# Optimization experiments

Measured on AMD Instinct MI355X. Metric: run time of the kernel, lower is better.

## Reference

```python
import jax, jax.numpy as jnp
import numpy as np

B, L, E, H, D = 4, 8192, 1024, 64, 2  # batch, seq, embed, heads, head_dim(=expand_ratio)
F_DIM = H * D  # forget_dim = 128
LOWER_BOUND = 0.0


def setup_inputs() -> dict:
    key = jax.random.key(0)
    k0, k1, k2, k3, k4 = jax.random.split(key, 5)
    s = E ** -0.5
    x = jax.random.normal(k0, (B, L, E), jnp.float32)
    Wq = jax.random.normal(k1, (E, F_DIM), jnp.float32) * s
    Wf = jax.random.normal(k2, (E, F_DIM), jnp.float32) * s
    Wi = jax.random.normal(k3, (E, F_DIM), jnp.float32) * s
    Wo = jax.random.normal(k4, (F_DIM, E), jnp.float32) * (F_DIM ** -0.5)
    return {"x": x, "Wq": Wq, "Wf": Wf, "Wi": Wi, "Wo": Wo}


def _split_heads(t):
    # b l (h d) -> b h l d
    return t.reshape(B, L, H, D).transpose(0, 2, 1, 3)


def _fused_recurrent_gla(q, k, v, g):
    # q,k,v,g: [b,h,l,d]; state S: [b,h,dk,dv]
    scale = D ** -0.5
    qs = jnp.moveaxis(q * scale, 2, 0)  # [l,b,h,d]
    ks = jnp.moveaxis(k, 2, 0)
    vs = jnp.moveaxis(v, 2, 0)
    gs = jnp.moveaxis(g, 2, 0)

    def step(S, inp):
        qt, kt, vt, gt = inp  # each [b,h,d]
        S = jnp.exp(gt)[..., None] * S + kt[..., None] * vt[..., None, :]
        o = jnp.einsum('bhk,bhkv->bhv', qt, S)
        return S, o

    S0 = jnp.zeros((B, H, D, D), q.dtype)
    _, o = jax.lax.scan(step, S0, (qs, ks, vs, gs))  # o: [l,b,h,d]
    return jnp.moveaxis(o, 0, 2)  # [b,h,l,d]


def reference(x, Wq, Wf, Wi, Wo):
    q = jax.nn.gelu(x @ Wq, approximate=False)  # torch nn.GELU default is exact erf
    f = x @ Wf
    g = LOWER_BOUND + (1.0 - LOWER_BOUND) * jax.nn.sigmoid(f)
    i = x @ Wi
    k = 1.0 - g
    g = jnp.log(g + 1e-6)
    q, k, v, g = map(_split_heads, (q, k, i, g))
    o = _fused_recurrent_gla(q, k, v, g)  # [b,h,l,d]
    o = o.transpose(0, 2, 1, 3).reshape(B, L, F_DIM)  # b h l d -> b l (h d)
    return jnp.tanh(o) @ Wo
```

## Files before the change

kernel.cpp:

```cpp
#include <hip/hip_runtime.h>
#include <hip/hip_bf16.h>


typedef __bf16 bf16x8 __attribute__((ext_vector_type(8)));
typedef float f32x4 __attribute__((ext_vector_type(4)));

__device__ __forceinline__ void async16(const void* g, void* l) {
  __builtin_amdgcn_global_load_lds(
      (const __attribute__((address_space(1))) unsigned int*)g,
      (__attribute__((address_space(3))) unsigned int*)l, 16, 0, 0);
}

__device__ __forceinline__ unsigned short f2bf(float f) {
  __hip_bfloat16 h = __float2bfloat16(f);
  return *reinterpret_cast<unsigned short*>(&h);
}
__device__ __forceinline__ float bf2f(unsigned short u) {
  union { unsigned int i; float f; } x; x.i = ((unsigned int)u) << 16; return x.f;
}

__global__ __launch_bounds__(256) void prep_w(
    const float* __restrict__ Wq, const float* __restrict__ Wf,
    const float* __restrict__ Wi, const float* __restrict__ Wo,
    unsigned short* __restrict__ WT, unsigned short* __restrict__ WoT) {
  int idx = blockIdx.x * 256 + threadIdx.x;
  if (idx < 393216) {
    int which = idx >> 17;
    int r = idx & 131071;
    int k = r >> 7, n = r & 127;
    const float* W = (which == 0) ? Wq : ((which == 1) ? Wf : Wi);
    WT[which * 131072 + n * 1024 + k] = f2bf(W[r]);
  } else {
    int r = idx - 393216;
    int k = r >> 10, n = r & 1023;
    WoT[n * 128 + k] = f2bf(Wo[r]);
  }
}

__global__ __launch_bounds__(256) void gemm1_kernel(
    const float* __restrict__ X, const unsigned short* __restrict__ WTall,
    unsigned short* __restrict__ qb, unsigned short* __restrict__ kb,
    unsigned short* __restrict__ vb, float* __restrict__ af) {
  __shared__ __align__(128) char smem[32768];
  const int t = threadIdx.x;
  const int lane = t & 63, w = t >> 6;
  const int quad = lane >> 4, c15 = lane & 15;
  const int wm = w >> 1, wn = w & 1;
  const int sel = blockIdx.x;
  const int row0 = blockIdx.y * 128;
  const unsigned short* Wt = WTall + (size_t)sel * 131072;

  const int lrow = t >> 3;
  const int ch = (t & 7) ^ (lrow & 7);
  const int ar = t >> 4;
  const int ac = (t & 15) >> 1;
  const int ah = t & 1;
  const int ak = (t & 15) * 4;

  f32x4 acc[4][4];
#pragma unroll
  for (int i = 0; i < 4; i++)
#pragma unroll
    for (int j = 0; j < 4; j++) acc[i][j] = (f32x4){0.f, 0.f, 0.f, 0.f};

  for (int kt = 0; kt < 16; ++kt) {
    float4 av[8];
#pragma unroll
    for (int i = 0; i < 8; ++i)
      av[i] = *(const float4*)(X + (size_t)(row0 + i * 16 + ar) * 1024 + kt * 64 + ak);
    __syncthreads();
#pragma unroll
    for (int c = 0; c < 4; ++c)
      async16(Wt + (size_t)(c * 32 + lrow) * 1024 + kt * 64 + ch * 8,
              smem + 16384 + c * 4096 + w * 1024);
#pragma unroll
    for (int i = 0; i < 8; ++i) {
      const int r = i * 16 + ar;
      short4 s4;
      s4.x = (short)f2bf(av[i].x); s4.y = (short)f2bf(av[i].y);
      s4.z = (short)f2bf(av[i].z); s4.w = (short)f2bf(av[i].w);
      *(short4*)(smem + r * 128 + ((ac ^ (r & 7)) << 4) + ah * 8) = s4;
    }
    __syncthreads();
#pragma unroll
    for (int ks = 0; ks < 2; ++ks) {
      bf16x8 afr[4], bfr[4];
      const int ck = ks * 4 + quad;
#pragma unroll
      for (int mi = 0; mi < 4; ++mi) {
        const int m = wm * 64 + mi * 16 + c15;
        afr[mi] = *(const bf16x8*)(smem + m * 128 + ((ck ^ (m & 7)) << 4));
      }
#pragma unroll
      for (int ni = 0; ni < 4; ++ni) {
        const int n = wn * 64 + ni * 16 + c15;
        bfr[ni] = *(const bf16x8*)(smem + 16384 + n * 128 + ((ck ^ (n & 7)) << 4));
      }
#pragma unroll
      for (int mi = 0; mi < 4; ++mi)
#pragma unroll
        for (int ni = 0; ni < 4; ++ni)
          acc[mi][ni] = __builtin_amdgcn_mfma_f32_16x16x32_bf16(afr[mi], bfr[ni], acc[mi][ni], 0, 0, 0);
    }
  }
#pragma unroll
  for (int mi = 0; mi < 4; ++mi) {
#pragma unroll
    for (int ni = 0; ni < 4; ++ni) {
#pragma unroll
      for (int r2 = 0; r2 < 4; ++r2) {
        float val = acc[mi][ni][r2];
        const int m = wm * 64 + mi * 16 + quad * 4 + r2;
        const int n = wn * 64 + ni * 16 + c15;
        const int grow = row0 + m;
        const int bb = grow >> 13, l = grow & 8191;
        const int h = n >> 1, d = n & 1;
        const size_t idx = (size_t)(bb * 64 + h) * 16384 + l * 2 + d;
        if (sel == 0) {
          qb[idx] = f2bf(0.5f * val * (1.f + erff(val * 0.70710678118654752f)));
        } else if (sel == 1) {
          float s  = 1.f / (1.f + expf(-val));
          float ks = 1.f / (1.f + expf(val));
          kb[idx] = f2bf(ks);
          af[idx] = s + 1e-6f;
        } else {
          vb[idx] = f2bf(val);
        }
      }
    }
  }
}

struct C6 { float A0, A1, B00, B01, B10, B11; };
__device__ __forceinline__ C6 comb(const C6& p, const C6& c) {
  C6 r;
  r.A0 = p.A0 * c.A0; r.A1 = p.A1 * c.A1;
  r.B00 = c.A0 * p.B00 + c.B00; r.B01 = c.A0 * p.B01 + c.B01;
  r.B10 = c.A1 * p.B10 + c.B10; r.B11 = c.A1 * p.B11 + c.B11;
  return r;
}
__device__ __forceinline__ C6 shflup(const C6& c, unsigned d) {
  C6 r;
  r.A0 = __shfl_up(c.A0, d); r.A1 = __shfl_up(c.A1, d);
  r.B00 = __shfl_up(c.B00, d); r.B01 = __shfl_up(c.B01, d);
  r.B10 = __shfl_up(c.B10, d); r.B11 = __shfl_up(c.B11, d);
  return r;
}
__device__ __forceinline__ void ld8bf(const unsigned short* p, float* dst) {
  union { int4 v; unsigned short u[8]; } x;
  x.v = *(const int4*)p;
#pragma unroll
  for (int j = 0; j < 8; ++j) dst[j] = bf2f(x.u[j]);
}

__global__ __launch_bounds__(256) void scan_kernel(
    const unsigned short* __restrict__ qb, const unsigned short* __restrict__ kb,
    const unsigned short* __restrict__ vb, const float* __restrict__ af,
    unsigned short* __restrict__ ob) {
  const int t = threadIdx.x, lane = t & 63, w = t >> 6;
  __shared__ C6 cw[2][4];
  const size_t base = (size_t)blockIdx.x * 16384;
  float P00 = 0.f, P01 = 0.f, P10 = 0.f, P11 = 0.f;

  for (int i = 0; i < 4; ++i) {
    const int e0 = i * 4096 + t * 16;
    float q[16], k[16], v[16], a[16];
    ld8bf(qb + base + e0, q); ld8bf(qb + base + e0 + 8, q + 8);
    ld8bf(kb + base + e0, k); ld8bf(kb + base + e0 + 8, k + 8);
    ld8bf(vb + base + e0, v); ld8bf(vb + base + e0 + 8, v + 8);
#pragma unroll
    for (int j = 0; j < 4; j++) ((float4*)a)[j] = ((const float4*)(af + base + e0))[j];

    C6 c = {1.f, 1.f, 0.f, 0.f, 0.f, 0.f};
#pragma unroll
    for (int j = 0; j < 8; j++) {
      float a0 = a[2 * j], a1 = a[2 * j + 1], k0 = k[2 * j], k1 = k[2 * j + 1];
      float v0 = v[2 * j], v1 = v[2 * j + 1];
      c.A0 *= a0; c.A1 *= a1;
      c.B00 = a0 * c.B00 + k0 * v0; c.B01 = a0 * c.B01 + k0 * v1;
      c.B10 = a1 * c.B10 + k1 * v0; c.B11 = a1 * c.B11 + k1 * v1;
    }
    C6 inc = c;
#pragma unroll
    for (int d = 1; d < 64; d <<= 1) {
      C6 u = shflup(inc, d);
      if (lane >= d) inc = comb(u, inc);
    }
    if (lane == 63) cw[i & 1][w] = inc;
    __syncthreads();
    C6 wp = {1.f, 1.f, 0.f, 0.f, 0.f, 0.f};
    for (int ww = 0; ww < w; ++ww) wp = comb(wp, cw[i & 1][ww]);
    C6 tot = cw[i & 1][0];
    for (int ww = 1; ww < 4; ++ww) tot = comb(tot, cw[i & 1][ww]);
    C6 ex = shflup(inc, 1);
    if (lane == 0) ex = (C6){1.f, 1.f, 0.f, 0.f, 0.f, 0.f};
    C6 te = comb(wp, ex);
    float S00 = te.A0 * P00 + te.B00, S01 = te.A0 * P01 + te.B01;
    float S10 = te.A1 * P10 + te.B10, S11 = te.A1 * P11 + te.B11;
    union { int4 v[2]; unsigned short u[16]; } ou;
#pragma unroll
    for (int j = 0; j < 8; j++) {
      float a0 = a[2 * j], a1 = a[2 * j + 1], k0 = k[2 * j], k1 = k[2 * j + 1];
      float v0 = v[2 * j], v1 = v[2 * j + 1];
      S00 = a0 * S00 + k0 * v0; S01 = a0 * S01 + k0 * v1;
      S10 = a1 * S10 + k1 * v0; S11 = a1 * S11 + k1 * v1;
      float o0 = 0.70710678118654752f * (q[2 * j] * S00 + q[2 * j + 1] * S10);
      float o1 = 0.70710678118654752f * (q[2 * j] * S01 + q[2 * j + 1] * S11);
      ou.u[2 * j] = f2bf(tanhf(o0));
      ou.u[2 * j + 1] = f2bf(tanhf(o1));
    }
    *(int4*)(ob + base + e0) = ou.v[0];
    *(int4*)(ob + base + e0 + 8) = ou.v[1];
    float nP00 = tot.A0 * P00 + tot.B00, nP01 = tot.A0 * P01 + tot.B01;
    float nP10 = tot.A1 * P10 + tot.B10, nP11 = tot.A1 * P11 + tot.B11;
    P00 = nP00; P01 = nP01; P10 = nP10; P11 = nP11;
  }
}

__global__ __launch_bounds__(256) void gemm2_kernel(
    const unsigned short* __restrict__ ob, const unsigned short* __restrict__ WoT,
    float* __restrict__ out) {
  __shared__ __align__(128) char smem[49152];
  const int t = threadIdx.x, lane = t & 63, w = t >> 6;
  const int quad = lane >> 4, c15 = lane & 15;
  const int n0 = blockIdx.x * 128;
  const int row0 = blockIdx.y * 64;
  const int bb = row0 >> 13;
  const int l0 = row0 & 8191;
  {
    const int h = t & 63, q2 = t >> 6;
    const unsigned short* g = ob + (size_t)(bb * 64 + h) * 16384 + (size_t)(l0 + q2 * 16) * 2;
    const int cbase = h >> 2;
    const int ioff = (h & 3) * 4;
#pragma unroll
    for (int i = 0; i < 4; i++) {
      union { int4 v; unsigned int u[4]; } d4;
      d4.v = *(const int4*)(g + i * 8);
#pragma unroll
      for (int jj = 0; jj < 4; jj++) {
        const int lrr = q2 * 16 + i * 4 + jj;
        *(unsigned int*)(smem + lrr * 256 + ((cbase ^ (lrr & 15)) << 4) + ioff) = d4.u[jj];
      }
    }
  }
  {
    const int rr = t >> 4;
    const int ch = (t & 15) ^ rr;
#pragma unroll
    for (int c = 0; c < 8; c++) {
      async16(WoT + (size_t)(n0 + c * 16 + rr) * 128 + ch * 8,
              smem + 16384 + c * 4096 + w * 1024);
    }
  }
  __syncthreads();
  f32x4 acc[4][2];
#pragma unroll
  for (int i = 0; i < 4; i++) { acc[i][0] = (f32x4){0.f,0.f,0.f,0.f}; acc[i][1] = (f32x4){0.f,0.f,0.f,0.f}; }
#pragma unroll
  for (int ks = 0; ks < 4; ++ks) {
    bf16x8 afr[4], bfr[2];
    const int ck = ks * 4 + quad;
#pragma unroll
    for (int mi = 0; mi < 4; ++mi) {
      const int m = mi * 16 + c15;
      afr[mi] = *(const bf16x8*)(smem + m * 256 + ((ck ^ (m & 15)) << 4));
    }
#pragma unroll
    for (int ni = 0; ni < 2; ++ni) {
      const int n = w * 32 + ni * 16 + c15;
      bfr[ni] = *(const bf16x8*)(smem + 16384 + n * 256 + ((ck ^ (n & 15)) << 4));
    }
#pragma unroll
    for (int mi = 0; mi < 4; ++mi)
#pragma unroll
      for (int ni = 0; ni < 2; ++ni)
        acc[mi][ni] = __builtin_amdgcn_mfma_f32_16x16x32_bf16(afr[mi], bfr[ni], acc[mi][ni], 0, 0, 0);
  }
#pragma unroll
  for (int mi = 0; mi < 4; ++mi)
#pragma unroll
    for (int ni = 0; ni < 2; ++ni)
#pragma unroll
      for (int r2 = 0; r2 < 4; ++r2) {
        const int m = mi * 16 + quad * 4 + r2;
        const int n = n0 + w * 32 + ni * 16 + c15;
        out[(size_t)(row0 + m) * 1024 + n] = acc[mi][ni][r2];
      }
}

extern "C" void kernel_launch(void* const* d_in, const int* in_sizes, int n_in,
                              void* d_out, int out_size, void* d_ws, size_t ws_size,
                              hipStream_t stream) {
  const float* x  = (const float*)d_in[0];
  const float* Wq = (const float*)d_in[1];
  const float* Wf = (const float*)d_in[2];
  const float* Wi = (const float*)d_in[3];
  const float* Wo = (const float*)d_in[4];
  float* out = (float*)d_out;
  char* ws = (char*)d_ws;

  unsigned short* WT  = (unsigned short*)(ws);
  unsigned short* WoT = (unsigned short*)(ws + 786432);
  unsigned short* qb  = (unsigned short*)(ws + 1048576);
  unsigned short* kb  = (unsigned short*)(ws + 1048576 + 8388608);
  unsigned short* vb  = (unsigned short*)(ws + 1048576 + 16777216);
  float*          af  = (float*)(ws + 1048576 + 25165824);
  unsigned short* ob  = (unsigned short*)(ws + 1048576 + 41943040);

  prep_w<<<2048, 256, 0, stream>>>(Wq, Wf, Wi, Wo, WT, WoT);
  gemm1_kernel<<<dim3(3, 256), 256, 0, stream>>>(x, WT, qb, kb, vb, af);
  scan_kernel<<<256, 256, 0, stream>>>(qb, kb, vb, af, ob);
  gemm2_kernel<<<dim3(8, 512), 256, 0, stream>>>(ob, WoT, out);
}
```

Baseline: 346.2 us.

## Fuse three projection GEMMs per block so X tile is loaded once

```diff
diff --git a/kernel.cpp b/kernel.cpp
--- a/kernel.cpp
+++ b/kernel.cpp
@@ -37,94 +37,104 @@
   }
 }
 
-__global__ __launch_bounds__(256) void gemm1_kernel(
+__global__ __launch_bounds__(256, 2) void gemm1_kernel(
     const float* __restrict__ X, const unsigned short* __restrict__ WTall,
     unsigned short* __restrict__ qb, unsigned short* __restrict__ kb,
     unsigned short* __restrict__ vb, float* __restrict__ af) {
-  __shared__ __align__(128) char smem[32768];
+  __shared__ __align__(128) char smem[57344];
   const int t = threadIdx.x;
   const int lane = t & 63, w = t >> 6;
   const int quad = lane >> 4, c15 = lane & 15;
   const int wm = w >> 1, wn = w & 1;
-  const int sel = blockIdx.x;
-  const int row0 = blockIdx.y * 128;
-  const unsigned short* Wt = WTall + (size_t)sel * 131072;
-
-  const int lrow = t >> 3;
-  const int ch = (t & 7) ^ (lrow & 7);
-  const int ar = t >> 4;
-  const int ac = (t & 15) >> 1;
-  const int ah = t & 1;
-  const int ak = (t & 15) * 4;
-
-  f32x4 acc[4][4];
-#pragma unroll
-  for (int i = 0; i < 4; i++)
-#pragma unroll
-    for (int j = 0; j < 4; j++) acc[i][j] = (f32x4){0.f, 0.f, 0.f, 0.f};
+  const int row0 = blockIdx.x * 64;
+
+  const int br = t >> 3;
+  const int bch = (t & 7) ^ (br & 7);
+  const int ar = t >> 2;
+  const int akf = (t & 3) * 16;
+  const int ac0 = (t & 3) * 2;
+
+  f32x4 acc[3][2][4];
+#pragma unroll
+  for (int s = 0; s < 3; ++s)
+#pragma unroll
+    for (int i = 0; i < 2; ++i)
+#pragma unroll
+      for (int j = 0; j < 4; ++j) acc[s][i][j] = (f32x4){0.f, 0.f, 0.f, 0.f};
 
   for (int kt = 0; kt < 16; ++kt) {
-    float4 av[8];
-#pragma unroll
-    for (int i = 0; i < 8; ++i)
-      av[i] = *(const float4*)(X + (size_t)(row0 + i * 16 + ar) * 1024 + kt * 64 + ak);
+    float4 av[4];
+    const float* xp = X + (size_t)(row0 + ar) * 1024 + kt * 64 + akf;
+#pragma unroll
+    for (int i = 0; i < 4; ++i) av[i] = *(const float4*)(xp + i * 4);
     __syncthreads();
 #pragma unroll
-    for (int c = 0; c < 4; ++c)
-      async16(Wt + (size_t)(c * 32 + lrow) * 1024 + kt * 64 + ch * 8,
-              smem + 16384 + c * 4096 + w * 1024);
-#pragma unroll
-    for (int i = 0; i < 8; ++i) {
-      const int r = i * 16 + ar;
-      short4 s4;
-      s4.x = (short)f2bf(av[i].x); s4.y = (short)f2bf(av[i].y);
-      s4.z = (short)f2bf(av[i].z); s4.w = (short)f2bf(av[i].w);
-      *(short4*)(smem + r * 128 + ((ac ^ (r & 7)) << 4) + ah * 8) = s4;
+    for (int s = 0; s < 3; ++s)
+#pragma unroll
+      for (int c = 0; c < 4; ++c)
+        async16(WTall + (size_t)s * 131072 + (size_t)(c * 32 + br) * 1024 + kt * 64 + bch * 8,
+                smem + 8192 + s * 16384 + c * 4096 + w * 1024);
+    {
+      union { unsigned short u[16]; int4 v[2]; } p;
+#pragma unroll
+      for (int i = 0; i < 4; ++i) {
+        p.u[4 * i + 0] = f2bf(av[i].x); p.u[4 * i + 1] = f2bf(av[i].y);
+        p.u[4 * i + 2] = f2bf(av[i].z); p.u[4 * i + 3] = f2bf(av[i].w);
+      }
+      *(int4*)(smem + ar * 128 + (((ac0 + 0) ^ (ar & 7)) << 4)) = p.v[0];
+      *(int4*)(smem + ar * 128 + (((ac0 + 1) ^ (ar & 7)) << 4)) = p.v[1];
     }
     __syncthreads();
 #pragma unroll
     for (int ks = 0; ks < 2; ++ks) {
-      bf16x8 afr[4], bfr[4];
       const int ck = ks * 4 + quad;
-#pragma unroll
-      for (int mi = 0; mi < 4; ++mi) {
-        const int m = wm * 64 + mi * 16 + c15;
+      bf16x8 afr[2], bfr[3][4];
+#pragma unroll
+      for (int mi = 0; mi < 2; ++mi) {
+        const int m = wm * 32 + mi * 16 + c15;
         afr[mi] = *(const bf16x8*)(smem + m * 128 + ((ck ^ (m & 7)) << 4));
       }
 #pragma unroll
+      for (int s = 0; s < 3; ++s)
+#pragma unroll
+        for (int ni = 0; ni < 4; ++ni) {
+          const int n = wn * 64 + ni * 16 + c15;
+          bfr[s][ni] = *(const bf16x8*)(smem + 8192 + s * 16384 + n * 128 + ((ck ^ (n & 7)) << 4));
+        }
+#pragma unroll
+      for (int s = 0; s < 3; ++s)
+#pragma unroll
+        for (int mi = 0; mi < 2; ++mi)
+#pragma unroll
+          for (int ni = 0; ni < 4; ++ni)
+            acc[s][mi][ni] = __builtin_amdgcn_mfma_f32_16x16x32_bf16(afr[mi], bfr[s][ni], acc[s][mi][ni], 0, 0, 0);
+    }
+  }
+#pragma unroll
+  for (int s = 0; s < 3; ++s) {
+#pragma unroll
+    for (int mi = 0; mi < 2; ++mi) {
+#pragma unroll
       for (int ni = 0; ni < 4; ++ni) {
-        const int n = wn * 64 + ni * 16 + c15;
-        bfr[ni] = *(const bf16x8*)(smem + 16384 + n * 128 + ((ck ^ (n & 7)) << 4));
-      }
-#pragma unroll
-      for (int mi = 0; mi < 4; ++mi)
-#pragma unroll
-        for (int ni = 0; ni < 4; ++ni)
-          acc[mi][ni] = __builtin_amdgcn_mfma_f32_16x16x32_bf16(afr[mi], bfr[ni], acc[mi][ni], 0, 0, 0);
-    }
-  }
-#pragma unroll
-  for (int mi = 0; mi < 4; ++mi) {
-#pragma unroll
-    for (int ni = 0; ni < 4; ++ni) {
-#pragma unroll
-      for (int r2 = 0; r2 < 4; ++r2) {
-        float val = acc[mi][ni][r2];
-        const int m = wm * 64 + mi * 16 + quad * 4 + r2;
-        const int n = wn * 64 + ni * 16 + c15;
-        const int grow = row0 + m;
-        const int bb = grow >> 13, l = grow & 8191;
-        const int h = n >> 1, d = n & 1;
-        const size_t idx = (size_t)(bb * 64 + h) * 16384 + l * 2 + d;
-        if (sel == 0) {
-          qb[idx] = f2bf(0.5f * val * (1.f + erff(val * 0.70710678118654752f)));
-        } else if (sel == 1) {
-          float s  = 1.f / (1.f + expf(-val));
-          float ks = 1.f / (1.f + expf(val));
-          kb[idx] = f2bf(ks);
-          af[idx] = s + 1e-6f;
-        } else {
-          vb[idx] = f2bf(val);
+#pragma unroll
+        for (int r2 = 0; r2 < 4; ++r2) {
+          float val = acc[s][mi][ni][r2];
+          const int m = wm * 32 + mi * 16 + quad * 4 + r2;
+          const int n = wn * 64 + ni * 16 + c15;
+          const int grow = row0 + m;
+          const int bb = grow >> 13, l = grow & 8191;
+          const int h = n >> 1, d = n & 1;
+          const size_t idx = (size_t)(bb * 64 + h) * 16384 + l * 2 + d;
+          if (s == 0) {
+            qb[idx] = f2bf(0.5f * val * (1.f + erff(val * 0.70710678118654752f)));
+          } else if (s == 1) {
+            float sg = 1.f / (1.f + expf(-val));
+            float ks = 1.f / (1.f + expf(val));
+            kb[idx] = f2bf(ks);
+            af[idx] = sg + 1e-6f;
+          } else {
+            vb[idx] = f2bf(val);
+          }
         }
       }
     }
@@ -308,7 +318,7 @@
   unsigned short* ob  = (unsigned short*)(ws + 1048576 + 41943040);
 
   prep_w<<<2048, 256, 0, stream>>>(Wq, Wf, Wi, Wo, WT, WoT);
-  gemm1_kernel<<<dim3(3, 256), 256, 0, stream>>>(x, WT, qb, kb, vb, af);
+  gemm1_kernel<<<512, 256, 0, stream>>>(x, WT, qb, kb, vb, af);
   scan_kernel<<<256, 256, 0, stream>>>(qb, kb, vb, af, ob);
   gemm2_kernel<<<dim3(8, 512), 256, 0, stream>>>(ob, WoT, out);
 }
```

New measurement: 314.5 us. 1.1x faster.
